# Optimization experiments

Hardware: AMD Instinct MI355X
Metric: run time of the kernel (lower is better)

## Reference

```python
import jax, jax.numpy as jnp
import numpy as np

B, S, H = 8, 2048, 1024  # batch, sqi_dim, hidden_dim


def setup_inputs() -> dict:
    key = jax.random.key(0)
    ks = jax.random.split(key, 10)
    lim_h = 1.0 / np.sqrt(H)
    lim_1 = 1.0  # Linear(1, H): fan_in = 1
    return {
        "hidden_states": jax.random.normal(ks[0], (B, S, H), dtype=jnp.float32),
        "sqi_sequence": jax.random.uniform(ks[1], (B, 1, S), dtype=jnp.float32),
        "pos_enc": jnp.zeros((1, S, H), dtype=jnp.float32),
        "Wq": jax.random.uniform(ks[2], (H, H), minval=-lim_h, maxval=lim_h),
        "bq": jax.random.uniform(ks[3], (H,), minval=-lim_h, maxval=lim_h),
        "Wk": jax.random.uniform(ks[4], (H, 1), minval=-lim_1, maxval=lim_1),
        "bk": jax.random.uniform(ks[5], (H,), minval=-lim_1, maxval=lim_1),
        "Wv": jax.random.uniform(ks[6], (H, H), minval=-lim_h, maxval=lim_h),
        "bv": jax.random.uniform(ks[7], (H,), minval=-lim_h, maxval=lim_h),
    }


def reference(hidden_states, sqi_sequence, pos_enc, Wq, bq, Wk, bk, Wv, bv):
    # hidden_states: [B, S, H]; sqi_sequence: [B, 1, S]
    x = hidden_states + pos_enc[:, :S, :]
    q = jnp.einsum("bsh,oh->bso", x, Wq) + bq                     # [B, S, H]
    sqi = jnp.transpose(sqi_sequence, (0, 2, 1))                   # [B, S, 1]
    k = sqi * Wk[:, 0] + bk                                        # Linear(1->H): [B, S, H]
    v = jnp.einsum("bsh,oh->bso", x, Wv) + bv                     # [B, S, H]
    scores = jnp.einsum("bqh,bkh->bqk", q, k) / jnp.sqrt(jnp.float32(H))
    attn = jax.nn.softmax(scores, axis=-1)                         # dropout = identity (eval)
    out = jnp.einsum("bqk,bkh->bqh", attn, v)                      # [B, S, H]
    context = jnp.mean(out, axis=1)                                # [B, H]
    return context, attn
```

## Files before the change

kernel.cpp:

```cpp
#include <hip/hip_runtime.h>
#include <math.h>

#define Bq 8
#define Sq 2048
#define Hq 1024
#define QT 16
#define INV_SQRT_H (1.0f / 32.0f)

typedef float f32x4 __attribute__((ext_vector_type(4)));

__device__ __forceinline__ float waveReduceSum(float v) {
#pragma unroll
    for (int off = 32; off > 0; off >>= 1) v += __shfl_xor(v, off, 64);
    return v;
}

__global__ void k_prep(const float* __restrict__ Wq, const float* __restrict__ Wk,
                       const float* __restrict__ bq, const float* __restrict__ sqi,
                       float* __restrict__ wq_eff, float* __restrict__ cb,
                       float* __restrict__ ext) {
    int bid = blockIdx.x, t = threadIdx.x;
    int wid = t >> 6, lane = t & 63;
    if (bid < 32) {
        int hc = bid & 3, oc = bid >> 2;
        int h = hc * 256 + t, o0 = oc * 128;
        float acc = 0.f;
#pragma unroll 4
        for (int o = 0; o < 128; ++o)
            acc += Wq[(size_t)(o0 + o) * Hq + h] * Wk[o0 + o];
        atomicAdd(&wq_eff[h], acc);
    } else if (bid == 32) {
        float acc = 0.f;
#pragma unroll
        for (int j = 0; j < 4; ++j) acc += bq[t * 4 + j] * Wk[t * 4 + j];
        acc = waveReduceSum(acc);
        __shared__ float red[4];
        if (lane == 0) red[wid] = acc;
        __syncthreads();
        if (t == 0) *cb = (red[0] + red[1] + red[2] + red[3]) * INV_SQRT_H;
    } else {
        int b = bid - 33;
        float mn = 1e30f, mx = -1e30f;
        for (int j = t; j < Sq; j += 256) {
            float v = sqi[b * Sq + j];
            mn = fminf(mn, v);
            mx = fmaxf(mx, v);
        }
#pragma unroll
        for (int off = 32; off > 0; off >>= 1) {
            mn = fminf(mn, __shfl_xor(mn, off, 64));
            mx = fmaxf(mx, __shfl_xor(mx, off, 64));
        }
        __shared__ float smn[4], smx[4];
        if (lane == 0) { smn[wid] = mn; smx[wid] = mx; }
        __syncthreads();
        if (t == 0) {
            ext[b]      = fminf(fminf(smn[0], smn[1]), fminf(smn[2], smn[3]));
            ext[Bq + b] = fmaxf(fmaxf(smx[0], smx[1]), fmaxf(smx[2], smx[3]));
        }
    }
}

__global__ void k_apos(const float* __restrict__ pos, const float* __restrict__ wq_eff,
                       float* __restrict__ apos) {
    int t = threadIdx.x, wid = t >> 6, lane = t & 63;
    int q0 = blockIdx.x * 16 + wid * 4;
    const float4* wp = (const float4*)wq_eff;
    float4 w0 = wp[lane], w1 = wp[lane + 64], w2 = wp[lane + 128], w3 = wp[lane + 192];
#pragma unroll
    for (int r = 0; r < 4; ++r) {
        const float4* pp = (const float4*)(pos + (size_t)(q0 + r) * Hq);
        float4 p0 = pp[lane], p1 = pp[lane + 64], p2 = pp[lane + 128], p3 = pp[lane + 192];
        float d = p0.x * w0.x + p0.y * w0.y + p0.z * w0.z + p0.w * w0.w
                + p1.x * w1.x + p1.y * w1.y + p1.z * w1.z + p1.w * w1.w
                + p2.x * w2.x + p2.y * w2.y + p2.z * w2.z + p2.w * w2.w
                + p3.x * w3.x + p3.y * w3.y + p3.z * w3.z + p3.w * w3.w;
        d = waveReduceSum(d);
        if (lane == 0) apos[q0 + r] = d * INV_SQRT_H;
    }
}

__global__ void __launch_bounds__(256) k_attn(
        const float* __restrict__ hidden, const float* __restrict__ apos,
        const float* __restrict__ wq_eff, const float* __restrict__ cbp,
        const float* __restrict__ sqi, const float* __restrict__ ext,
        float* __restrict__ attn, float* __restrict__ wcol) {
    int b = blockIdx.y, qt = blockIdx.x, t = threadIdx.x;
    int wid = t >> 6, lane = t & 63;
    __shared__ float sqi_s[Sq];
    __shared__ float colsum[Sq];
    {
        const float4* sp = (const float4*)(sqi + b * Sq);
        float4* ds = (float4*)sqi_s;
        ds[t]       = sp[t];
        ds[256 + t] = sp[256 + t];
    }
    float smin = ext[b], smax = ext[Bq + b];
    float cbv = *cbp;

    const float4* wp = (const float4*)wq_eff;
    float4 w0 = wp[lane], w1 = wp[lane + 64], w2 = wp[lane + 128], w3 = wp[lane + 192];
    int q0 = qt * QT + wid * 4;
    float a[4];
#pragma unroll
    for (int r = 0; r < 4; ++r) {
        const float4* hp = (const float4*)(hidden + (size_t)(b * Sq + q0 + r) * Hq);
        float4 h0 = hp[lane], h1 = hp[lane + 64], h2 = hp[lane + 128], h3 = hp[lane + 192];
        float d = h0.x * w0.x + h0.y * w0.y + h0.z * w0.z + h0.w * w0.w
                + h1.x * w1.x + h1.y * w1.y + h1.z * w1.z + h1.w * w1.w
                + h2.x * w2.x + h2.y * w2.y + h2.z * w2.z + h2.w * w2.w
                + h3.x * w3.x + h3.y * w3.y + h3.z * w3.z + h3.w * w3.w;
        d = waveReduceSum(d);
        a[r] = d * INV_SQRT_H + apos[q0 + r] + cbv;
    }
    __syncthreads();

    const float4* ss = (const float4*)sqi_s;
    float4 ca[8];
#pragma unroll
    for (int c = 0; c < 8; ++c) ca[c] = make_float4(0.f, 0.f, 0.f, 0.f);

#pragma unroll
    for (int r = 0; r < 4; ++r) {
        float aa = a[r];
        float m = (aa > 0.f) ? aa * smax : aa * smin;
        float4 e[8];
        float s = 0.f;
#pragma unroll
        for (int c = 0; c < 8; ++c) {
            float4 sv = ss[lane + 64 * c];
            e[c].x = __expf(aa * sv.x - m);
            e[c].y = __expf(aa * sv.y - m);
            e[c].z = __expf(aa * sv.z - m);
            e[c].w = __expf(aa * sv.w - m);
            s += e[c].x + e[c].y + e[c].z + e[c].w;
        }
        s = waveReduceSum(s);
        float rinv = 1.0f / s;
        f32x4* orow = (f32x4*)(attn + (size_t)(b * Sq + q0 + r) * Sq);
#pragma unroll
        for (int c = 0; c < 8; ++c) {
            f32x4 p;
            p.x = e[c].x * rinv; p.y = e[c].y * rinv;
            p.z = e[c].z * rinv; p.w = e[c].w * rinv;
            __builtin_nontemporal_store(p, &orow[lane + 64 * c]);
            ca[c].x += p.x; ca[c].y += p.y; ca[c].z += p.z; ca[c].w += p.w;
        }
    }

    float4* cs = (float4*)colsum;
    if (wid == 0) {
#pragma unroll
        for (int c = 0; c < 8; ++c) cs[lane + 64 * c] = ca[c];
    }
    __syncthreads();
#pragma unroll
    for (int w = 1; w < 4; ++w) {
        if (wid == w) {
#pragma unroll
            for (int c = 0; c < 8; ++c) {
                float4 v = cs[lane + 64 * c];
                v.x += ca[c].x; v.y += ca[c].y; v.z += ca[c].z; v.w += ca[c].w;
                cs[lane + 64 * c] = v;
            }
        }
        __syncthreads();
    }
#pragma unroll
    for (int j = 0; j < 8; ++j)
        atomicAdd(&wcol[b * Sq + j * 256 + t], colsum[j * 256 + t]);
}

__global__ void k_y(const float* __restrict__ hidden, const float* __restrict__ pos,
                    const float* __restrict__ wcol, float* __restrict__ y) {
    int b = blockIdx.y, kc = blockIdx.x, t = threadIdx.x;
    int kk0 = kc * (Sq / 32);
    float4 acc = {0, 0, 0, 0};
    for (int i = 0; i < Sq / 32; ++i) {
        int kk = kk0 + i;
        float wv = wcol[b * Sq + kk] * (1.0f / Sq);
        float4 hv = ((const float4*)(hidden + ((size_t)(b * Sq + kk)) * Hq))[t];
        float4 pv = ((const float4*)(pos + (size_t)kk * Hq))[t];
        acc.x += wv * (hv.x + pv.x);
        acc.y += wv * (hv.y + pv.y);
        acc.z += wv * (hv.z + pv.z);
        acc.w += wv * (hv.w + pv.w);
    }
    atomicAdd(&y[b * Hq + t * 4 + 0], acc.x);
    atomicAdd(&y[b * Hq + t * 4 + 1], acc.y);
    atomicAdd(&y[b * Hq + t * 4 + 2], acc.z);
    atomicAdd(&y[b * Hq + t * 4 + 3], acc.w);
}

__global__ void k_ctx(const float* __restrict__ Wv, const float* __restrict__ bv,
                      const float* __restrict__ y, float* __restrict__ ctx) {
    int b = blockIdx.y, kc = blockIdx.z, t = threadIdx.x;
    int h = blockIdx.x * 256 + t;
    __shared__ float ys[256];
    ys[t] = y[b * Hq + kc * 256 + t];
    __syncthreads();
    const float4* wrow = (const float4*)(Wv + (size_t)h * Hq + kc * 256);
    float acc = 0.f;
#pragma unroll 8
    for (int j = 0; j < 64; ++j) {
        float4 w4 = wrow[j];
        acc += w4.x * ys[j * 4 + 0] + w4.y * ys[j * 4 + 1] +
               w4.z * ys[j * 4 + 2] + w4.w * ys[j * 4 + 3];
    }
    if (kc == 0) acc += bv[h];
    atomicAdd(&ctx[b * Hq + h], acc);
}

extern "C" void kernel_launch(void* const* d_in, const int* in_sizes, int n_in,
                              void* d_out, int out_size, void* d_ws, size_t ws_size,
                              hipStream_t stream) {
    const float* hidden = (const float*)d_in[0];
    const float* sqi    = (const float*)d_in[1];
    const float* pos    = (const float*)d_in[2];
    const float* Wq     = (const float*)d_in[3];
    const float* bq     = (const float*)d_in[4];
    const float* Wk     = (const float*)d_in[5];
    const float* Wv     = (const float*)d_in[7];
    const float* bv     = (const float*)d_in[8];

    float* out  = (float*)d_out;
    float* ctx  = out;
    float* attn = out + Bq * Hq;

    float* ws     = (float*)d_ws;
    float* wq_eff = ws;
    float* wcol   = ws + 1024;
    float* y      = ws + 17408;
    float* ext    = ws + 25600;
    float* cb     = ws + 25616;
    float* apos   = ws + 25632;

    (void)hipMemsetAsync(ws, 0, 25600 * sizeof(float), stream);
    (void)hipMemsetAsync(ctx, 0, Bq * Hq * sizeof(float), stream);

    k_prep<<<41, 256, 0, stream>>>(Wq, Wk, bq, sqi, wq_eff, cb, ext);
    k_apos<<<Sq / 16, 256, 0, stream>>>(pos, wq_eff, apos);
    k_attn<<<dim3(Sq / QT, Bq), 256, 0, stream>>>(hidden, apos, wq_eff, cb,
                                                  sqi, ext, attn, wcol);
    k_y   <<<dim3(32, Bq), 256, 0, stream>>>(hidden, pos, wcol, y);
    k_ctx <<<dim3(Hq / 256, Bq, 4), 256, 0, stream>>>(Wv, bv, y, ctx);
}
```

Before: 259.5 us.

## Fuse pos projection into attention, widen query tiles, restructure y and ctx kernels

Drops the separate k_apos kernel and adds pos directly to hidden inside k_attn's dot product. Each attention block now handles 32 queries (8 per wave) and reduces column sums with LDS atomics instead of a serialized per-wave pass, which halves the global atomics into wcol. k_y gets twice as many blocks with shorter loops, and k_ctx becomes a one-wave-per-row dot product with a wave reduction, removing the ctx memset and its global atomics. The cost is re-reading pos for every batch inside k_attn and higher register pressure from the larger tile.

```diff
diff --git a/kernel.cpp b/kernel.cpp
--- a/kernel.cpp
+++ b/kernel.cpp
@@ -4,7 +4,7 @@
 #define Bq 8
 #define Sq 2048
 #define Hq 1024
-#define QT 16
+#define QT 32
 #define INV_SQRT_H (1.0f / 32.0f)
 
 typedef float f32x4 __attribute__((ext_vector_type(4)));
@@ -61,27 +61,8 @@
     }
 }
 
-__global__ void k_apos(const float* __restrict__ pos, const float* __restrict__ wq_eff,
-                       float* __restrict__ apos) {
-    int t = threadIdx.x, wid = t >> 6, lane = t & 63;
-    int q0 = blockIdx.x * 16 + wid * 4;
-    const float4* wp = (const float4*)wq_eff;
-    float4 w0 = wp[lane], w1 = wp[lane + 64], w2 = wp[lane + 128], w3 = wp[lane + 192];
-#pragma unroll
-    for (int r = 0; r < 4; ++r) {
-        const float4* pp = (const float4*)(pos + (size_t)(q0 + r) * Hq);
-        float4 p0 = pp[lane], p1 = pp[lane + 64], p2 = pp[lane + 128], p3 = pp[lane + 192];
-        float d = p0.x * w0.x + p0.y * w0.y + p0.z * w0.z + p0.w * w0.w
-                + p1.x * w1.x + p1.y * w1.y + p1.z * w1.z + p1.w * w1.w
-                + p2.x * w2.x + p2.y * w2.y + p2.z * w2.z + p2.w * w2.w
-                + p3.x * w3.x + p3.y * w3.y + p3.z * w3.z + p3.w * w3.w;
-        d = waveReduceSum(d);
-        if (lane == 0) apos[q0 + r] = d * INV_SQRT_H;
-    }
-}
-
 __global__ void __launch_bounds__(256) k_attn(
-        const float* __restrict__ hidden, const float* __restrict__ apos,
+        const float* __restrict__ hidden, const float* __restrict__ pos,
         const float* __restrict__ wq_eff, const float* __restrict__ cbp,
         const float* __restrict__ sqi, const float* __restrict__ ext,
         float* __restrict__ attn, float* __restrict__ wcol) {
@@ -94,24 +75,29 @@
         float4* ds = (float4*)sqi_s;
         ds[t]       = sp[t];
         ds[256 + t] = sp[256 + t];
+        float4* cz = (float4*)colsum;
+        cz[t]       = make_float4(0.f, 0.f, 0.f, 0.f);
+        cz[256 + t] = make_float4(0.f, 0.f, 0.f, 0.f);
     }
     float smin = ext[b], smax = ext[Bq + b];
     float cbv = *cbp;
 
     const float4* wp = (const float4*)wq_eff;
     float4 w0 = wp[lane], w1 = wp[lane + 64], w2 = wp[lane + 128], w3 = wp[lane + 192];
-    int q0 = qt * QT + wid * 4;
-    float a[4];
-#pragma unroll
-    for (int r = 0; r < 4; ++r) {
+    int q0 = qt * QT + wid * 8;
+    float a[8];
+#pragma unroll
+    for (int r = 0; r < 8; ++r) {
         const float4* hp = (const float4*)(hidden + (size_t)(b * Sq + q0 + r) * Hq);
+        const float4* pp = (const float4*)(pos + (size_t)(q0 + r) * Hq);
         float4 h0 = hp[lane], h1 = hp[lane + 64], h2 = hp[lane + 128], h3 = hp[lane + 192];
-        float d = h0.x * w0.x + h0.y * w0.y + h0.z * w0.z + h0.w * w0.w
-                + h1.x * w1.x + h1.y * w1.y + h1.z * w1.z + h1.w * w1.w
-                + h2.x * w2.x + h2.y * w2.y + h2.z * w2.z + h2.w * w2.w
-                + h3.x * w3.x + h3.y * w3.y + h3.z * w3.z + h3.w * w3.w;
+        float4 p0 = pp[lane], p1 = pp[lane + 64], p2 = pp[lane + 128], p3 = pp[lane + 192];
+        float d = (h0.x + p0.x) * w0.x + (h0.y + p0.y) * w0.y + (h0.z + p0.z) * w0.z + (h0.w + p0.w) * w0.w
+                + (h1.x + p1.x) * w1.x + (h1.y + p1.y) * w1.y + (h1.z + p1.z) * w1.z + (h1.w + p1.w) * w1.w
+                + (h2.x + p2.x) * w2.x + (h2.y + p2.y) * w2.y + (h2.z + p2.z) * w2.z + (h2.w + p2.w) * w2.w
+                + (h3.x + p3.x) * w3.x + (h3.y + p3.y) * w3.y + (h3.z + p3.z) * w3.z + (h3.w + p3.w) * w3.w;
         d = waveReduceSum(d);
-        a[r] = d * INV_SQRT_H + apos[q0 + r] + cbv;
+        a[r] = d * INV_SQRT_H + cbv;
     }
     __syncthreads();
 
@@ -120,8 +106,7 @@
 #pragma unroll
     for (int c = 0; c < 8; ++c) ca[c] = make_float4(0.f, 0.f, 0.f, 0.f);
 
-#pragma unroll
-    for (int r = 0; r < 4; ++r) {
+    for (int r = 0; r < 8; ++r) {
         float aa = a[r];
         float m = (aa > 0.f) ? aa * smax : aa * smin;
         float4 e[8];
@@ -148,24 +133,15 @@
         }
     }
 
-    float4* cs = (float4*)colsum;
-    if (wid == 0) {
-#pragma unroll
-        for (int c = 0; c < 8; ++c) cs[lane + 64 * c] = ca[c];
+#pragma unroll
+    for (int c = 0; c < 8; ++c) {
+        int base = (lane + 64 * c) * 4;
+        atomicAdd(&colsum[base + 0], ca[c].x);
+        atomicAdd(&colsum[base + 1], ca[c].y);
+        atomicAdd(&colsum[base + 2], ca[c].z);
+        atomicAdd(&colsum[base + 3], ca[c].w);
     }
     __syncthreads();
-#pragma unroll
-    for (int w = 1; w < 4; ++w) {
-        if (wid == w) {
-#pragma unroll
-            for (int c = 0; c < 8; ++c) {
-                float4 v = cs[lane + 64 * c];
-                v.x += ca[c].x; v.y += ca[c].y; v.z += ca[c].z; v.w += ca[c].w;
-                cs[lane + 64 * c] = v;
-            }
-        }
-        __syncthreads();
-    }
 #pragma unroll
     for (int j = 0; j < 8; ++j)
         atomicAdd(&wcol[b * Sq + j * 256 + t], colsum[j * 256 + t]);
@@ -174,9 +150,10 @@
 __global__ void k_y(const float* __restrict__ hidden, const float* __restrict__ pos,
                     const float* __restrict__ wcol, float* __restrict__ y) {
     int b = blockIdx.y, kc = blockIdx.x, t = threadIdx.x;
-    int kk0 = kc * (Sq / 32);
+    int kk0 = kc * 32;
     float4 acc = {0, 0, 0, 0};
-    for (int i = 0; i < Sq / 32; ++i) {
+#pragma unroll 4
+    for (int i = 0; i < 32; ++i) {
         int kk = kk0 + i;
         float wv = wcol[b * Sq + kk] * (1.0f / Sq);
         float4 hv = ((const float4*)(hidden + ((size_t)(b * Sq + kk)) * Hq))[t];
@@ -194,21 +171,25 @@
 
 __global__ void k_ctx(const float* __restrict__ Wv, const float* __restrict__ bv,
                       const float* __restrict__ y, float* __restrict__ ctx) {
-    int b = blockIdx.y, kc = blockIdx.z, t = threadIdx.x;
-    int h = blockIdx.x * 256 + t;
-    __shared__ float ys[256];
-    ys[t] = y[b * Hq + kc * 256 + t];
+    int b = blockIdx.y, t = threadIdx.x;
+    int wid = t >> 6, lane = t & 63;
+    __shared__ float4 ys4[Hq / 4];
+    ys4[t] = ((const float4*)(y + b * Hq))[t];
     __syncthreads();
-    const float4* wrow = (const float4*)(Wv + (size_t)h * Hq + kc * 256);
-    float acc = 0.f;
-#pragma unroll 8
-    for (int j = 0; j < 64; ++j) {
-        float4 w4 = wrow[j];
-        acc += w4.x * ys[j * 4 + 0] + w4.y * ys[j * 4 + 1] +
-               w4.z * ys[j * 4 + 2] + w4.w * ys[j * 4 + 3];
-    }
-    if (kc == 0) acc += bv[h];
-    atomicAdd(&ctx[b * Hq + h], acc);
+    float4 y0 = ys4[lane], y1 = ys4[lane + 64], y2 = ys4[lane + 128], y3 = ys4[lane + 192];
+    int h0 = blockIdx.x * 16 + wid * 4;
+#pragma unroll
+    for (int r = 0; r < 4; ++r) {
+        int h = h0 + r;
+        const float4* wrow = (const float4*)(Wv + (size_t)h * Hq);
+        float4 v0 = wrow[lane], v1 = wrow[lane + 64], v2 = wrow[lane + 128], v3 = wrow[lane + 192];
+        float d = v0.x * y0.x + v0.y * y0.y + v0.z * y0.z + v0.w * y0.w
+                + v1.x * y1.x + v1.y * y1.y + v1.z * y1.z + v1.w * y1.w
+                + v2.x * y2.x + v2.y * y2.y + v2.z * y2.z + v2.w * y2.w
+                + v3.x * y3.x + v3.y * y3.y + v3.z * y3.z + v3.w * y3.w;
+        d = waveReduceSum(d);
+        if (lane == 0) ctx[b * Hq + h] = d + bv[h];
+    }
 }
 
 extern "C" void kernel_launch(void* const* d_in, const int* in_sizes, int n_in,
@@ -233,15 +214,12 @@
     float* y      = ws + 17408;
     float* ext    = ws + 25600;
     float* cb     = ws + 25616;
-    float* apos   = ws + 25632;
 
     (void)hipMemsetAsync(ws, 0, 25600 * sizeof(float), stream);
-    (void)hipMemsetAsync(ctx, 0, Bq * Hq * sizeof(float), stream);
 
     k_prep<<<41, 256, 0, stream>>>(Wq, Wk, bq, sqi, wq_eff, cb, ext);
-    k_apos<<<Sq / 16, 256, 0, stream>>>(pos, wq_eff, apos);
-    k_attn<<<dim3(Sq / QT, Bq), 256, 0, stream>>>(hidden, apos, wq_eff, cb,
+    k_attn<<<dim3(Sq / QT, Bq), 256, 0, stream>>>(hidden, pos, wq_eff, cb,
                                                   sqi, ext, attn, wcol);
-    k_y   <<<dim3(32, Bq), 256, 0, stream>>>(hidden, pos, wcol, y);
-    k_ctx <<<dim3(Hq / 256, Bq, 4), 256, 0, stream>>>(Wv, bv, y, ctx);
-}
+    k_y   <<<dim3(64, Bq), 256, 0, stream>>>(hidden, pos, wcol, y);
+    k_ctx <<<dim3(Hq / 16, Bq), 256, 0, stream>>>(Wv, bv, y, ctx);
+}
```

Measured after the change: 268.2 us. +3.3%, slower.
